# Kernel optimization log

Hardware: AMD Instinct MI355X
Metric: run time of the kernel (lower is better)

Reference implementation:

```python
import jax, jax.numpy as jnp
import numpy as np

B, T, C = 4, 2048, 1024
H_DIM = 1024
N_HEADS = 16
MAX_T = 2048


def setup_inputs() -> dict:
    key = jax.random.key(0)
    ks = jax.random.split(key, 9)
    s = 1.0 / np.sqrt(C)
    return {
        "x": jax.random.normal(ks[0], (B, T, C), dtype=jnp.float32),
        "Wq": jax.random.normal(ks[1], (C, H_DIM), dtype=jnp.float32) * s,
        "bq": jnp.zeros((H_DIM,), dtype=jnp.float32),
        "Wk": jax.random.normal(ks[2], (C, H_DIM), dtype=jnp.float32) * s,
        "bk": jnp.zeros((H_DIM,), dtype=jnp.float32),
        "Wv": jax.random.normal(ks[3], (C, H_DIM), dtype=jnp.float32) * s,
        "bv": jnp.zeros((H_DIM,), dtype=jnp.float32),
        "Wo": jax.random.normal(ks[4], (H_DIM, H_DIM), dtype=jnp.float32) * s,
        "bo": jnp.zeros((H_DIM,), dtype=jnp.float32),
    }


def reference(x, Wq, bq, Wk, bk, Wv, bv, Wo, bo):
    Bx, Tx, Cx = x.shape
    N = N_HEADS
    D = Cx // N
    # QKV projections -> (B, N, T, D)
    q = (x @ Wq + bq).reshape(Bx, Tx, N, D).transpose(0, 2, 1, 3)
    k = (x @ Wk + bk).reshape(Bx, Tx, N, D).transpose(0, 2, 1, 3)
    v = (x @ Wv + bv).reshape(Bx, Tx, N, D).transpose(0, 2, 1, 3)
    # causal scores (B, N, T, T)
    scores = jnp.einsum('bntd,bnfd->bntf', q, k) / jnp.sqrt(jnp.asarray(D, x.dtype))
    causal = jnp.tril(jnp.ones((Tx, Tx), dtype=bool))[None, None]
    scores = jnp.where(causal, scores, -jnp.inf)
    normalized_weights = jax.nn.softmax(scores, axis=-1)
    attention = jnp.einsum('bntf,bnfd->bntd', normalized_weights, v)
    attention = attention.transpose(0, 2, 1, 3).reshape(Bx, Tx, N * D)
    out = attention @ Wo + bo
    return out, normalized_weights
```

## Files before the change

kernel.cpp:

```cpp
#include <hip/hip_runtime.h>

typedef unsigned short UST;
typedef __bf16 v8bf __attribute__((ext_vector_type(8)));
typedef float  v4f  __attribute__((ext_vector_type(4)));

__device__ __forceinline__ UST f2b(float f) {
  union { float f; unsigned u; } x; x.f = f;
  unsigned u = x.u;
  unsigned r = (u + 0x7fffu + ((u >> 16) & 1u)) >> 16;
  return (UST)r;
}

__device__ __forceinline__ float fexp2(float x) {
  return __builtin_amdgcn_exp2f(x);
}

typedef __attribute__((address_space(3))) unsigned lds_u;
typedef __attribute__((address_space(1))) const unsigned glb_u;
__device__ __forceinline__ void gl_lds16(const UST* g, UST* s) {
  __builtin_amdgcn_global_load_lds((glb_u*)g, (lds_u*)s, 16, 0, 0);
}

__global__ __launch_bounds__(256) void k_convert(const float* __restrict__ src,
                                                 UST* __restrict__ dst, int n) {
  int i = (blockIdx.x * 256 + threadIdx.x) * 4;
  if (i >= n) return;
  float4 v = *(const float4*)(src + i);
  ushort4 o;
  o.x = f2b(v.x); o.y = f2b(v.y); o.z = f2b(v.z); o.w = f2b(v.w);
  *(ushort4*)(dst + i) = o;
}

__global__ __launch_bounds__(256) void k_transpose(const float* __restrict__ W,
                                                   UST* __restrict__ WT, int R, int C) {
  __shared__ float tile[32][33];
  int tx = threadIdx.x, ty = threadIdx.y;
  int r0 = blockIdx.y * 32, c0 = blockIdx.x * 32;
  for (int i = ty; i < 32; i += 8)
    tile[i][tx] = W[(size_t)(r0 + i) * C + c0 + tx];
  __syncthreads();
  for (int i = ty; i < 32; i += 8)
    WT[(size_t)(c0 + i) * R + r0 + tx] = f2b(tile[tx][i]);
}

__global__ __launch_bounds__(256) void k_gemm_bt(const UST* __restrict__ A,
                                                 const UST* __restrict__ BT,
                                                 const float* __restrict__ bias,
                                                 int M, int N, int K, int mode,
                                                 void* __restrict__ outp) {
  __shared__ UST As[128 * 32];
  __shared__ UST Bs[128 * 32];
  int tid = threadIdx.x;
  int l = tid & 63, w = tid >> 6;
  int g = l >> 4, c16 = l & 15;
  int wm = w >> 1, wn = w & 1;
  int bm = blockIdx.y * 128, bn = blockIdx.x * 128;

  int ch0 = tid, ch1 = tid + 256;
  const UST* a0p = A + (size_t)(bm + (ch0 >> 2)) * K + (ch0 & 3) * 8;
  const UST* a1p = A + (size_t)(bm + (ch1 >> 2)) * K + (ch1 & 3) * 8;
  const UST* b0p = BT + (size_t)(bn + (ch0 >> 2)) * K + (ch0 & 3) * 8;
  const UST* b1p = BT + (size_t)(bn + (ch1 >> 2)) * K + (ch1 & 3) * 8;

  v4f acc[4][4];
  for (int i = 0; i < 4; i++)
    for (int j = 0; j < 4; j++)
      acc[i][j] = (v4f){0.f, 0.f, 0.f, 0.f};

  for (int kb = 0; kb < K; kb += 32) {
    __syncthreads();
    gl_lds16(a0p + kb, As + (size_t)ch0 * 8);
    gl_lds16(a1p + kb, As + (size_t)ch1 * 8);
    gl_lds16(b0p + kb, Bs + (size_t)ch0 * 8);
    gl_lds16(b1p + kb, Bs + (size_t)ch1 * 8);
    __syncthreads();

    v8bf af[4], bf[4];
    for (int mt = 0; mt < 4; mt++)
      af[mt] = *(const v8bf*)(As + (wm * 64 + mt * 16 + c16) * 32 + g * 8);
    for (int nt = 0; nt < 4; nt++)
      bf[nt] = *(const v8bf*)(Bs + (wn * 64 + nt * 16 + c16) * 32 + g * 8);
    for (int mt = 0; mt < 4; mt++)
      for (int nt = 0; nt < 4; nt++)
        acc[mt][nt] = __builtin_amdgcn_mfma_f32_16x16x32_bf16(af[mt], bf[nt], acc[mt][nt], 0, 0, 0);
  }

  for (int mt = 0; mt < 4; mt++)
    for (int nt = 0; nt < 4; nt++)
      for (int r = 0; r < 4; r++) {
        int row = bm + wm * 64 + mt * 16 + g * 4 + r;
        int col = bn + wn * 64 + nt * 16 + c16;
        float v = acc[mt][nt][r] + bias[col];
        if (mode == 1) {
          int b = row >> 11, t = row & 2047, hn = col >> 6, d = col & 63;
          ((UST*)outp)[((size_t)((b * 16 + hn) * 2048 + t)) * 64 + d] = f2b(v);
        } else if (mode == 2) {
          int b = row >> 11, t = row & 2047, hn = col >> 6, d = col & 63;
          ((UST*)outp)[((size_t)((b * 16 + hn) * 64 + d)) * 2048 + t] = f2b(v);
        } else {
          ((float*)outp)[(size_t)row * N + col] = v;
        }
      }
}

__global__ __launch_bounds__(256) void k_attn(const UST* __restrict__ qh,
                                              const UST* __restrict__ kh,
                                              const UST* __restrict__ vT,
                                              float* __restrict__ Pout,
                                              UST* __restrict__ oh) {
  __shared__ UST Ks[2][64 * 64];
  __shared__ UST Pt[4][16 * 32];

  int tid = threadIdx.x;
  int l = tid & 63, w = tid >> 6, g = l >> 4, c16 = l & 15;
  int qt = blockIdx.x, hn = blockIdx.y, b = blockIdx.z;

  const UST* qbase = qh + ((size_t)((b * 16 + hn) * 2048 + qt * 64)) * 64;
  const UST* kbase = kh + ((size_t)((b * 16 + hn) * 2048)) * 64;
  const UST* vbase = vT + ((size_t)((b * 16 + hn) * 64)) * 2048;
  float* pbase = Pout + ((size_t)((b * 16 + hn) * 2048 + qt * 64)) * 2048;

  const float SC = 0.18033688011f;

  v8bf aq0 = *(const v8bf*)(qbase + (size_t)(w * 16 + c16) * 64 + g * 8);
  v8bf aq1 = *(const v8bf*)(qbase + (size_t)(w * 16 + c16) * 64 + 32 + g * 8);

  int r0 = tid >> 3, cb = tid & 7;
  const UST* ksrc0 = kbase + (size_t)r0 * 64 + (size_t)((cb ^ (r0 & 7)) * 8);
  const UST* ksrc1 = kbase + (size_t)(r0 + 32) * 64 + (size_t)((cb ^ ((r0 + 32) & 7)) * 8);
  auto stageK = [&](int ib, int c) {
    gl_lds16(ksrc0 + (size_t)c * 4096, &Ks[ib][(size_t)tid * 8]);
    gl_lds16(ksrc1 + (size_t)c * 4096, &Ks[ib][(size_t)(tid + 256) * 8]);
  };

  int qrow_base = qt * 64 + w * 16 + g * 4;
  int sw = c16 & 7;

  float lL[4] = {0.f, 0.f, 0.f, 0.f};

  stageK(0, 0);
  for (int c = 0; c <= qt; c++) {
    int ib = c & 1;
    int cn = (c < qt) ? c + 1 : qt;
    stageK(ib ^ 1, cn);
    asm volatile("s_waitcnt vmcnt(2)" ::: "memory");
    __builtin_amdgcn_s_barrier();
    __builtin_amdgcn_sched_barrier(0);
    for (int ft = 0; ft < 4; ft++) {
      v8bf b0 = *(const v8bf*)(&Ks[ib][(size_t)(ft * 16 + c16) * 64 + ((g ^ sw) * 8)]);
      v8bf b1 = *(const v8bf*)(&Ks[ib][(size_t)(ft * 16 + c16) * 64 + (((4 + g) ^ sw) * 8)]);
      v4f s = (v4f){0.f, 0.f, 0.f, 0.f};
      s = __builtin_amdgcn_mfma_f32_16x16x32_bf16(aq0, b0, s, 0, 0, 0);
      s = __builtin_amdgcn_mfma_f32_16x16x32_bf16(aq1, b1, s, 0, 0, 0);
      int f = c * 64 + ft * 16 + c16;
      for (int r = 0; r < 4; r++) {
        float e = fexp2(s[r] * SC);
        lL[r] += (f <= qrow_base + r) ? e : 0.f;
      }
    }
    __builtin_amdgcn_sched_barrier(0);
    __builtin_amdgcn_s_barrier();
  }
  asm volatile("s_waitcnt vmcnt(0)" ::: "memory");
  __builtin_amdgcn_s_barrier();

  stageK(0, 0);
  float rl[4];
  for (int r = 0; r < 4; r++) {
    float t = lL[r];
    for (int d = 1; d < 16; d <<= 1) t += __shfl_xor(t, d);
    rl[r] = 1.f / t;
  }

  v4f accO[4];
  for (int nt = 0; nt < 4; nt++) accO[nt] = (v4f){0.f, 0.f, 0.f, 0.f};

  for (int c = 0; c <= qt; c++) {
    int ib = c & 1;
    int cn = (c < qt) ? c + 1 : qt;
    stageK(ib ^ 1, cn);
    asm volatile("s_waitcnt vmcnt(2)" ::: "memory");
    __builtin_amdgcn_s_barrier();
    __builtin_amdgcn_sched_barrier(0);
    for (int fp = 0; fp < 2; fp++) {
      for (int t2 = 0; t2 < 2; t2++) {
        int ft = fp * 2 + t2;
        v8bf b0 = *(const v8bf*)(&Ks[ib][(size_t)(ft * 16 + c16) * 64 + ((g ^ sw) * 8)]);
        v8bf b1 = *(const v8bf*)(&Ks[ib][(size_t)(ft * 16 + c16) * 64 + (((4 + g) ^ sw) * 8)]);
        v4f s = (v4f){0.f, 0.f, 0.f, 0.f};
        s = __builtin_amdgcn_mfma_f32_16x16x32_bf16(aq0, b0, s, 0, 0, 0);
        s = __builtin_amdgcn_mfma_f32_16x16x32_bf16(aq1, b1, s, 0, 0, 0);
        int f = c * 64 + ft * 16 + c16;
        for (int r = 0; r < 4; r++) {
          bool ok = f <= (qrow_base + r);
          float pv = ok ? fexp2(s[r] * SC) * rl[r] : 0.f;
          pbase[(size_t)(w * 16 + g * 4 + r) * 2048 + f] = pv;
          Pt[w][(g * 4 + r) * 32 + t2 * 16 + c16] = f2b(pv);
        }
      }
      v8bf pa = *(const v8bf*)(&Pt[w][c16 * 32 + g * 8]);
      for (int nt = 0; nt < 4; nt++) {
        const UST* vp = vbase + (size_t)(nt * 16 + c16) * 2048 + c * 64 + fp * 32 + g * 8;
        v8bf vb = *(const v8bf*)vp;
        accO[nt] = __builtin_amdgcn_mfma_f32_16x16x32_bf16(pa, vb, accO[nt], 0, 0, 0);
      }
    }
    __builtin_amdgcn_sched_barrier(0);
    __builtin_amdgcn_s_barrier();
  }
  asm volatile("s_waitcnt vmcnt(0)" ::: "memory");

  {
    float4 z4 = make_float4(0.f, 0.f, 0.f, 0.f);
    for (int c = qt + 1; c < 32; c++) {
      float4* zp = (float4*)(pbase + (size_t)(w * 16 + (l >> 2)) * 2048 + c * 64) + (l & 3);
      zp[0] = z4; zp[4] = z4; zp[8] = z4; zp[12] = z4;
    }
  }

  for (int nt = 0; nt < 4; nt++)
    for (int r = 0; r < 4; r++) {
      int qrow = qt * 64 + w * 16 + g * 4 + r;
      int col = hn * 64 + nt * 16 + c16;
      oh[(size_t)(b * 2048 + qrow) * 1024 + col] = f2b(accO[nt][r]);
    }
}

extern "C" void kernel_launch(void* const* d_in, const int* in_sizes, int n_in,
                              void* d_out, int out_size, void* d_ws, size_t ws_size,
                              hipStream_t stream) {
  const float* x  = (const float*)d_in[0];
  const float* Wq = (const float*)d_in[1];
  const float* bq = (const float*)d_in[2];
  const float* Wk = (const float*)d_in[3];
  const float* bk = (const float*)d_in[4];
  const float* Wv = (const float*)d_in[5];
  const float* bv = (const float*)d_in[6];
  const float* Wo = (const float*)d_in[7];
  const float* bo = (const float*)d_in[8];

  float* out  = (float*)d_out;
  float* Pout = out + 8388608;

  UST* xb  = (UST*)d_ws;
  UST* wqT = xb  + 8388608;
  UST* wkT = wqT + 1048576;
  UST* wvT = wkT + 1048576;
  UST* woT = wvT + 1048576;
  UST* qhp = woT + 1048576;
  UST* khp = qhp + 8388608;
  UST* vTp = khp + 8388608;
  UST* ohp = vTp + 8388608;

  k_convert<<<8192, 256, 0, stream>>>(x, xb, 8388608);
  dim3 tb(32, 8), tg(32, 32);
  k_transpose<<<tg, tb, 0, stream>>>(Wq, wqT, 1024, 1024);
  k_transpose<<<tg, tb, 0, stream>>>(Wk, wkT, 1024, 1024);
  k_transpose<<<tg, tb, 0, stream>>>(Wv, wvT, 1024, 1024);
  k_transpose<<<tg, tb, 0, stream>>>(Wo, woT, 1024, 1024);

  dim3 gg(8, 64);
  k_gemm_bt<<<gg, 256, 0, stream>>>(xb, wqT, bq, 8192, 1024, 1024, 1, qhp);
  k_gemm_bt<<<gg, 256, 0, stream>>>(xb, wkT, bk, 8192, 1024, 1024, 1, khp);
  k_gemm_bt<<<gg, 256, 0, stream>>>(xb, wvT, bv, 8192, 1024, 1024, 2, vTp);

  dim3 ag(32, 16, 4);
  k_attn<<<ag, 256, 0, stream>>>(qhp, khp, vTp, Pout, ohp);

  k_gemm_bt<<<gg, 256, 0, stream>>>(ohp, woT, bo, 8192, 1024, 1024, 3, d_out);
}
```

Measured before the change: 2.199 ms.

## Transpose score MFMA so each lane owns a query row; vectorize P stores

Swaps the MFMA operand order so each lane holds four consecutive key columns of one query row. The fp32 probability matrix can then be written as 16-byte nontemporal vector stores instead of scalar strided stores, and the row-sum reduction shrinks to two shuffles. The P staging buffer in LDS is padded to a 40-element stride and written as packed bf16 pairs to avoid bank conflicts. The vmcnt wait is loosened to let V loads and P stores stay in flight across iterations, which risks being wrong if the count of outstanding operations does not match.

```diff
diff --git a/kernel.cpp b/kernel.cpp
--- a/kernel.cpp
+++ b/kernel.cpp
@@ -109,7 +109,7 @@
                                               float* __restrict__ Pout,
                                               UST* __restrict__ oh) {
   __shared__ UST Ks[2][64 * 64];
-  __shared__ UST Pt[4][16 * 32];
+  __shared__ UST Pt[4][16 * 40];
 
   int tid = threadIdx.x;
   int l = tid & 63, w = tid >> 6, g = l >> 4, c16 = l & 15;
@@ -133,10 +133,10 @@
     gl_lds16(ksrc1 + (size_t)c * 4096, &Ks[ib][(size_t)(tid + 256) * 8]);
   };
 
-  int qrow_base = qt * 64 + w * 16 + g * 4;
+  int qrow = qt * 64 + w * 16 + c16;
   int sw = c16 & 7;
 
-  float lL[4] = {0.f, 0.f, 0.f, 0.f};
+  float lsum = 0.f;
 
   stageK(0, 0);
   for (int c = 0; c <= qt; c++) {
@@ -150,12 +150,12 @@
       v8bf b0 = *(const v8bf*)(&Ks[ib][(size_t)(ft * 16 + c16) * 64 + ((g ^ sw) * 8)]);
       v8bf b1 = *(const v8bf*)(&Ks[ib][(size_t)(ft * 16 + c16) * 64 + (((4 + g) ^ sw) * 8)]);
       v4f s = (v4f){0.f, 0.f, 0.f, 0.f};
-      s = __builtin_amdgcn_mfma_f32_16x16x32_bf16(aq0, b0, s, 0, 0, 0);
-      s = __builtin_amdgcn_mfma_f32_16x16x32_bf16(aq1, b1, s, 0, 0, 0);
-      int f = c * 64 + ft * 16 + c16;
+      s = __builtin_amdgcn_mfma_f32_16x16x32_bf16(b0, aq0, s, 0, 0, 0);
+      s = __builtin_amdgcn_mfma_f32_16x16x32_bf16(b1, aq1, s, 0, 0, 0);
+      int f0 = c * 64 + ft * 16 + g * 4;
       for (int r = 0; r < 4; r++) {
         float e = fexp2(s[r] * SC);
-        lL[r] += (f <= qrow_base + r) ? e : 0.f;
+        lsum += (f0 + r <= qrow) ? e : 0.f;
       }
     }
     __builtin_amdgcn_sched_barrier(0);
@@ -165,12 +165,10 @@
   __builtin_amdgcn_s_barrier();
 
   stageK(0, 0);
-  float rl[4];
-  for (int r = 0; r < 4; r++) {
-    float t = lL[r];
-    for (int d = 1; d < 16; d <<= 1) t += __shfl_xor(t, d);
-    rl[r] = 1.f / t;
-  }
+  float t = lsum;
+  t += __shfl_xor(t, 16);
+  t += __shfl_xor(t, 32);
+  float rl = 1.f / t;
 
   v4f accO[4];
   for (int nt = 0; nt < 4; nt++) accO[nt] = (v4f){0.f, 0.f, 0.f, 0.f};
@@ -179,7 +177,8 @@
     int ib = c & 1;
     int cn = (c < qt) ? c + 1 : qt;
     stageK(ib ^ 1, cn);
-    asm volatile("s_waitcnt vmcnt(2)" ::: "memory");
+    if (c == 0) { asm volatile("s_waitcnt vmcnt(2)" ::: "memory"); }
+    else        { asm volatile("s_waitcnt vmcnt(14)" ::: "memory"); }
     __builtin_amdgcn_s_barrier();
     __builtin_amdgcn_sched_barrier(0);
     for (int fp = 0; fp < 2; fp++) {
@@ -188,17 +187,25 @@
         v8bf b0 = *(const v8bf*)(&Ks[ib][(size_t)(ft * 16 + c16) * 64 + ((g ^ sw) * 8)]);
         v8bf b1 = *(const v8bf*)(&Ks[ib][(size_t)(ft * 16 + c16) * 64 + (((4 + g) ^ sw) * 8)]);
         v4f s = (v4f){0.f, 0.f, 0.f, 0.f};
-        s = __builtin_amdgcn_mfma_f32_16x16x32_bf16(aq0, b0, s, 0, 0, 0);
-        s = __builtin_amdgcn_mfma_f32_16x16x32_bf16(aq1, b1, s, 0, 0, 0);
-        int f = c * 64 + ft * 16 + c16;
-        for (int r = 0; r < 4; r++) {
-          bool ok = f <= (qrow_base + r);
-          float pv = ok ? fexp2(s[r] * SC) * rl[r] : 0.f;
-          pbase[(size_t)(w * 16 + g * 4 + r) * 2048 + f] = pv;
-          Pt[w][(g * 4 + r) * 32 + t2 * 16 + c16] = f2b(pv);
-        }
-      }
-      v8bf pa = *(const v8bf*)(&Pt[w][c16 * 32 + g * 8]);
+        s = __builtin_amdgcn_mfma_f32_16x16x32_bf16(b0, aq0, s, 0, 0, 0);
+        s = __builtin_amdgcn_mfma_f32_16x16x32_bf16(b1, aq1, s, 0, 0, 0);
+        int f0 = c * 64 + ft * 16 + g * 4;
+        v4f pv;
+        pv[0] = (f0 + 0 <= qrow) ? fexp2(s[0] * SC) * rl : 0.f;
+        pv[1] = (f0 + 1 <= qrow) ? fexp2(s[1] * SC) * rl : 0.f;
+        pv[2] = (f0 + 2 <= qrow) ? fexp2(s[2] * SC) * rl : 0.f;
+        pv[3] = (f0 + 3 <= qrow) ? fexp2(s[3] * SC) * rl : 0.f;
+        __builtin_nontemporal_store(pv,
+            (v4f*)(pbase + (size_t)(w * 16 + c16) * 2048 + f0));
+        union { __bf16 h[2]; unsigned u; } p01, p23;
+        p01.h[0] = (__bf16)pv[0]; p01.h[1] = (__bf16)pv[1];
+        p23.h[0] = (__bf16)pv[2]; p23.h[1] = (__bf16)pv[3];
+        unsigned* pt32 = (unsigned*)(&Pt[w][0]);
+        int b32 = c16 * 20 + t2 * 8 + g * 2;
+        pt32[b32] = p01.u;
+        pt32[b32 + 1] = p23.u;
+      }
+      v8bf pa = *(const v8bf*)(&Pt[w][c16 * 40 + g * 8]);
       for (int nt = 0; nt < 4; nt++) {
         const UST* vp = vbase + (size_t)(nt * 16 + c16) * 2048 + c * 64 + fp * 32 + g * 8;
         v8bf vb = *(const v8bf*)vp;
@@ -211,18 +218,21 @@
   asm volatile("s_waitcnt vmcnt(0)" ::: "memory");
 
   {
-    float4 z4 = make_float4(0.f, 0.f, 0.f, 0.f);
+    v4f z4 = (v4f){0.f, 0.f, 0.f, 0.f};
     for (int c = qt + 1; c < 32; c++) {
-      float4* zp = (float4*)(pbase + (size_t)(w * 16 + (l >> 2)) * 2048 + c * 64) + (l & 3);
-      zp[0] = z4; zp[4] = z4; zp[8] = z4; zp[12] = z4;
+      v4f* zp = (v4f*)(pbase + (size_t)(w * 16 + (l >> 2)) * 2048 + c * 64) + (l & 3);
+      __builtin_nontemporal_store(z4, zp + 0);
+      __builtin_nontemporal_store(z4, zp + 4);
+      __builtin_nontemporal_store(z4, zp + 8);
+      __builtin_nontemporal_store(z4, zp + 12);
     }
   }
 
   for (int nt = 0; nt < 4; nt++)
     for (int r = 0; r < 4; r++) {
-      int qrow = qt * 64 + w * 16 + g * 4 + r;
+      int qr = qt * 64 + w * 16 + g * 4 + r;
       int col = hn * 64 + nt * 16 + c16;
-      oh[(size_t)(b * 2048 + qrow) * 1024 + col] = f2b(accO[nt][r]);
+      oh[(size_t)(b * 2048 + qr) * 1024 + col] = f2b(accO[nt][r]);
     }
 }
 
```

New measurement: 2.097 ms. 1.05x faster.
